# Kernel optimization log

Hardware: AMD Instinct MI355X
Metric: run time of the kernel (lower is better)

## Reference

```python
import jax, jax.numpy as jnp
import numpy as np

B, S, D = 8, 4096, 1024
E = 64            # num_experts
K = 2             # top-k
CAP_F = 1.25      # capacity_factor
TEMP = 0.1        # temperature buffer
Z_COEF = 1e-4
LB_COEF = 1e-4


def setup_inputs() -> dict:
    key = jax.random.key(0)
    kx, k1, k2 = jax.random.split(key, 3)
    x = jax.random.normal(kx, (B, S, D), dtype=jnp.float32)
    W1 = jax.random.normal(k1, (D, D // 2), dtype=jnp.float32) * 0.02
    ln_gamma = jnp.ones((D // 2,), dtype=jnp.float32)
    ln_beta = jnp.zeros((D // 2,), dtype=jnp.float32)
    W2 = jax.random.normal(k2, (D // 2, E), dtype=jnp.float32) * 0.02
    return {"x": x, "W1": W1, "ln_gamma": ln_gamma, "ln_beta": ln_beta, "W2": W2}


def _router_logits(x2, W1, ln_gamma, ln_beta, W2):
    h = x2 @ W1                                   # [T, D//2]
    mu = h.mean(-1, keepdims=True)
    var = h.var(-1, keepdims=True)                # biased var, as torch LayerNorm
    h = (h - mu) / jnp.sqrt(var + 1e-5) * ln_gamma + ln_beta
    h = jax.nn.relu(h)
    logits = h @ W2                               # [T, E]
    logits = jnp.clip(logits, -50.0, 50.0)
    nrm = jnp.linalg.norm(logits, axis=-1, keepdims=True)
    return logits / (jnp.maximum(nrm, 1e-6) + 1e-6)


def reference(x, W1, ln_gamma, ln_beta, W2):
    T = x.shape[0] * x.shape[1]
    x2 = x.reshape(T, -1)
    logits = _router_logits(x2, W1, ln_gamma, ln_beta, W2)   # [T, E]
    routing_weights = jax.nn.softmax(logits / TEMP, axis=-1)

    # top-k + weight renormalization (no_grad in original)
    tw, ti = jax.lax.top_k(routing_weights, K)               # [T, K]
    tw = jnp.clip(tw, 1e-3, 0.8)
    tw = tw / (jnp.maximum(tw.sum(-1, keepdims=True), 1e-6) + 1e-6)
    tw = jax.lax.stop_gradient(tw)
    ti = jax.lax.stop_gradient(ti)

    capacity = CAP_F * T * K / E
    counts = jnp.zeros((E,), dtype=jnp.float32)
    dispatch = jnp.zeros((T, E), dtype=jnp.float32)
    rows = jnp.arange(T)
    for kk in range(K):  # fixed small loop over k, matches sequential scatter semantics
        e = ti[:, kk]                                        # [T] expert ids
        m = counts[e] < capacity                             # capacity check vs pre-step counts
        counts = counts + jax.ops.segment_sum(m.astype(jnp.float32), e, num_segments=E)
        cur = dispatch[rows, e]
        dispatch = dispatch.at[rows, e].set(jnp.where(m, tw[:, kk], cur))

    unrouted = dispatch.sum(-1) == 0                         # [T]
    least_loaded = jnp.argmax(capacity - counts)
    dispatch = jnp.where(unrouted[:, None] & (jnp.arange(E) == least_loaded)[None, :], 1.0, dispatch)
    ndm = dispatch / jnp.maximum(dispatch.sum(-1, keepdims=True), 1e-12)
    ndm = jax.lax.stop_gradient(ndm)

    # training losses
    lp = jnp.clip(jax.nn.log_softmax(logits, axis=-1), -50.0, 50.0)
    z_loss = jnp.minimum(jnp.mean(lp * lp), 100.0)
    usage = ndm.sum(0)
    usage = usage / (jnp.maximum(usage.sum(), 1e-6) + 1e-6)
    usage = jnp.clip(usage, 1e-6, 1.0)
    target = jnp.full((E,), 1.0 / E, dtype=jnp.float32)
    # F.kl_div(log(usage+1e-6), target, reduction='batchmean') on 1-D -> divide by E
    kl = jnp.sum(target * (jnp.log(target) - jnp.log(usage + 1e-6))) / E
    kl = jnp.minimum(kl, 100.0)
    loss = Z_COEF * z_loss + LB_COEF * kl
    loss = jnp.where(jnp.isnan(loss) | jnp.isinf(loss), jnp.float32(0.1), loss)

    return jax.lax.stop_gradient(routing_weights), ndm, loss
```

## Files before the change

### kernel.cpp

```cpp
#include <hip/hip_runtime.h>
#include <hip/hip_bf16.h>
#include <math.h>

#define T_TOK 32768
#define D_IN  1024
#define H_DIM 512
#define N_E   64
#define TM    32
#define BK    16
#define CAPACITY 1280
#define MARGIN   2e-4f
#define MARGIN_F 1e-4f
#define KC1 384

#define WS_H    0ull
#define WS_W1P  67108864ull
#define WS_OFF  69206016ull
#define WS_NEED 69900000ull
#define WS_TI0 0
#define WS_TI1 (4*T_TOK)
#define WS_TW0 (8*T_TOK)
#define WS_TW1 (12*T_TOK)
#define WS_CNT (16*T_TOK)
#define WS_USG (WS_CNT+256)
#define WS_FLAGN (WS_USG+256)
#define WS_ZP  (WS_FLAGN+256)
#define WS_FLAGL (WS_ZP+4096)

typedef __attribute__((ext_vector_type(8))) short short8;
typedef __attribute__((ext_vector_type(4))) float f32x4;

__device__ __forceinline__ float wred64(float v){
#pragma unroll
  for (int m=1;m<64;m<<=1) v += __shfl_xor(v, m, 64);
  return v;
}
__device__ __forceinline__ unsigned short f2bf(float f){
  union { __hip_bfloat16 h; unsigned short u; } cv;
  cv.h = __float2bfloat16(f);
  return cv.u;
}
__device__ __forceinline__ float bf2f(unsigned short u){
  union { __hip_bfloat16 h; unsigned short u; } cv;
  cv.u = u;
  return __bfloat162float(cv.h);
}

__device__ __forceinline__ float np_sum8acc(const float* a, int n){
  float r0=a[0],r1=a[1],r2=a[2],r3=a[3],r4=a[4],r5=a[5],r6=a[6],r7=a[7];
  int lim = n - (n & 7);
  int i = 8;
  for (; i < lim; i += 8){
    r0=__fadd_rn(r0,a[i]);   r1=__fadd_rn(r1,a[i+1]);
    r2=__fadd_rn(r2,a[i+2]); r3=__fadd_rn(r3,a[i+3]);
    r4=__fadd_rn(r4,a[i+4]); r5=__fadd_rn(r5,a[i+5]);
    r6=__fadd_rn(r6,a[i+6]); r7=__fadd_rn(r7,a[i+7]);
  }
  float res=__fadd_rn(__fadd_rn(__fadd_rn(r0,r1),__fadd_rn(r2,r3)),
                      __fadd_rn(__fadd_rn(r4,r5),__fadd_rn(r6,r7)));
  for (; i < n; ++i) res=__fadd_rn(res,a[i]);
  return res;
}
__device__ __forceinline__ float np_sum512(const float* a){
  float s01=__fadd_rn(np_sum8acc(a,128),     np_sum8acc(a+128,128));
  float s23=__fadd_rn(np_sum8acc(a+256,128), np_sum8acc(a+384,128));
  return __fadd_rn(s01,s23);
}

__global__ void k_pack(const float* __restrict__ W1, unsigned short* __restrict__ W1p)
{
  int T = blockIdx.x*256 + threadIdx.x;
  int lane = T & 63;  int rest = T >> 6;
  int nt = rest & 7;  rest >>= 3;
  int s  = rest & 1;  rest >>= 1;
  int ks = rest & 31; int nb = rest >> 5;
  int n  = nb*128 + nt*16 + (lane & 15);
  int kb = ks*32 + (lane >> 4)*8;
  unsigned short o[8];
#pragma unroll
  for (int j=0;j<8;++j){
    float w = W1[(size_t)(kb+j)*H_DIM + n];
    unsigned short hi = f2bf(w);
    o[j] = s ? f2bf(w - bf2f(hi)) : hi;
  }
  size_t base = ((size_t)((((nb*32+ks)*2+s)*8+nt))*512 + (size_t)lane*8);
#pragma unroll
  for (int j=0;j<8;++j) W1p[base+j] = o[j];
}

__launch_bounds__(256)
__global__ void k_g1(const float* __restrict__ x, const unsigned short* __restrict__ W1p,
                     float* __restrict__ h)
{
  __shared__ __align__(16) unsigned short aF[2][8192];
  __shared__ __align__(16) unsigned short bF[2][8192];

  int b = blockIdx.x;
  int logical = (b & 7)*128 + (b >> 3);
  const int nbn = logical >> 8;
  const int bm  = logical & 255;
  const int t0  = bm * 128;

  const int tid  = threadIdx.x;
  const int lane = tid & 63;
  const int wid  = tid >> 6;
  const int wr4  = (wid >> 1) * 4;
  const int wc4  = (wid & 1) * 4;
  const int kq    = tid & 7;
  const int rbase = tid >> 3;
  const int alane = (rbase & 15) + 16*(kq>>1);
  const int j4 = (kq & 1)*4;

  f32x4 acc[4][4];
#pragma unroll
  for (int m=0;m<4;++m)
#pragma unroll
    for (int n=0;n<4;++n) acc[m][n] = (f32x4){0.f,0.f,0.f,0.f};

  {
    float4 xa[4]; uint4 bb[4];
#pragma unroll
    for (int i=0;i<4;++i)
      xa[i] = *(const float4*)&x[(size_t)(t0 + rbase + 32*i)*D_IN + kq*4];
    size_t chunk = (size_t)(nbn*32 + 0) * 8192;
#pragma unroll
    for (int i=0;i<4;++i)
      bb[i] = *(const uint4*)&W1p[chunk + (size_t)(i*256+tid)*8];
#pragma unroll
    for (int i=0;i<4;++i){
      int mt = (rbase + 32*i) >> 4;
      ushort4 uh, ul;
      uh.x=f2bf(xa[i].x); ul.x=f2bf(xa[i].x - bf2f(uh.x));
      uh.y=f2bf(xa[i].y); ul.y=f2bf(xa[i].y - bf2f(uh.y));
      uh.z=f2bf(xa[i].z); ul.z=f2bf(xa[i].z - bf2f(uh.z));
      uh.w=f2bf(xa[i].w); ul.w=f2bf(xa[i].w - bf2f(uh.w));
      *(ushort4*)&aF[0][(mt*64+alane)*8 + j4]        = uh;
      *(ushort4*)&aF[0][4096 + (mt*64+alane)*8 + j4] = ul;
    }
#pragma unroll
    for (int i=0;i<4;++i)
      *(uint4*)&bF[0][(i*256+tid)*8] = bb[i];
  }

  int cur = 0;
  for (int ks=0; ks<32; ++ks){
    __syncthreads();
    float4 xa[4]; uint4 bb[4];
    const bool pre = (ks+1 < 32);
    if (pre){
      int k1 = (ks+1)*32;
#pragma unroll
      for (int i=0;i<4;++i)
        xa[i] = *(const float4*)&x[(size_t)(t0 + rbase + 32*i)*D_IN + k1 + kq*4];
      size_t chunk = (size_t)(nbn*32 + (ks+1)) * 8192;
#pragma unroll
      for (int i=0;i<4;++i)
        bb[i] = *(const uint4*)&W1p[chunk + (size_t)(i*256+tid)*8];
    }
    short8 ah[4], al[4], bh[4], bl[4];
#pragma unroll
    for (int m=0;m<4;++m){
      ah[m] = *(const short8*)&aF[cur][((wr4+m)*64+lane)*8];
      al[m] = *(const short8*)&aF[cur][4096 + ((wr4+m)*64+lane)*8];
    }
#pragma unroll
    for (int n=0;n<4;++n){
      bh[n] = *(const short8*)&bF[cur][((wc4+n)*64+lane)*8];
      bl[n] = *(const short8*)&bF[cur][4096 + ((wc4+n)*64+lane)*8];
    }
#pragma unroll
    for (int m=0;m<4;++m)
#pragma unroll
      for (int n=0;n<4;++n){
        acc[m][n] = __builtin_amdgcn_mfma_f32_16x16x32_bf16(ah[m], bh[n], acc[m][n], 0,0,0);
        acc[m][n] = __builtin_amdgcn_mfma_f32_16x16x32_bf16(al[m], bh[n], acc[m][n], 0,0,0);
        acc[m][n] = __builtin_amdgcn_mfma_f32_16x16x32_bf16(ah[m], bl[n], acc[m][n], 0,0,0);
      }
    if (pre){
      int nb_ = cur ^ 1;
#pragma unroll
      for (int i=0;i<4;++i){
        int mt = (rbase + 32*i) >> 4;
        ushort4 uh, ul;
        uh.x=f2bf(xa[i].x); ul.x=f2bf(xa[i].x - bf2f(uh.x));
        uh.y=f2bf(xa[i].y); ul.y=f2bf(xa[i].y - bf2f(uh.y));
        uh.z=f2bf(xa[i].z); ul.z=f2bf(xa[i].z - bf2f(uh.z));
        uh.w=f2bf(xa[i].w); ul.w=f2bf(xa[i].w - bf2f(uh.w));
        *(ushort4*)&aF[nb_][(mt*64+alane)*8 + j4]        = uh;
        *(ushort4*)&aF[nb_][4096 + (mt*64+alane)*8 + j4] = ul;
      }
#pragma unroll
      for (int i=0;i<4;++i)
        *(uint4*)&bF[nb_][(i*256+tid)*8] = bb[i];
    }
    cur ^= 1;
  }

  const int cr = (lane >> 4) * 4;
  const int cc = lane & 15;
#pragma unroll
  for (int m=0;m<4;++m)
#pragma unroll
    for (int n=0;n<4;++n){
      int row0 = t0 + (wr4+m)*16 + cr;
      int col  = nbn*128 + (wc4+n)*16 + cc;
#pragma unroll
      for (int r=0;r<4;++r)
        h[(size_t)(row0+r)*H_DIM + col] = acc[m][n][r];
    }
}

__launch_bounds__(256, 3)
__global__ void k_ln2(const float* __restrict__ h,
                      const float* __restrict__ gamma,
                      const float* __restrict__ beta,
                      const float* __restrict__ W2,
                      float* __restrict__ out_rw,
                      int*   __restrict__ ti0, int* __restrict__ ti1,
                      float* __restrict__ tw0, float* __restrict__ tw1,
                      float* __restrict__ zpart,
                      int* __restrict__ flagn, int* __restrict__ flagl)
{
  __shared__ __align__(16) char smem[53888];
  __shared__ float zw[4];
  float* hnT  = (float*)smem;
  float* redS = (float*)(smem + 36864);
  float* redQ = (float*)(smem + 36864 + 4224);
  float* sW2  = (float*)(smem + 36864);
  float* logitsL = (float*)(smem + 45312);
  float* muA  = (float*)(smem + 53632);
  float* rsA  = (float*)(smem + 53760);

  const int tid  = threadIdx.x;
  const int wv   = tid >> 6;
  const int lane = tid & 63;
  const int tl   = lane & 7;
  const int cl   = lane >> 3;
  const int cbase = wv*128 + cl*16;
  const int t0 = blockIdx.x * TM;

  float acc[4][16];
#pragma unroll
  for (int j=0;j<4;++j)
#pragma unroll
    for (int q=0;q<4;++q)
      *(float4*)&acc[j][q*4] = *(const float4*)&h[(size_t)(t0+tl*4+j)*H_DIM + cbase + q*4];

  const int g = wv*8 + cl;
#pragma unroll
  for (int j=0;j<4;++j) {
    float s=0.f, qq=0.f;
#pragma unroll
    for (int q=0;q<16;++q){ s += acc[j][q]; qq += acc[j][q]*acc[j][q]; }
    redS[(tl*4+j)*33 + g] = s;
    redQ[(tl*4+j)*33 + g] = qq;
  }
  __syncthreads();
  if (tid < 32) {
    float s=0.f, qq=0.f;
    for (int gg=0; gg<32; ++gg){ s += redS[tid*33+gg]; qq += redQ[tid*33+gg]; }
    float mu = s * (1.f/512.f);
    float var = qq * (1.f/512.f) - mu*mu;
    muA[tid] = mu;
    rsA[tid] = rsqrtf(var + 1e-5f);
  }
  __syncthreads();

  {
    float gmv[16], btv[16];
#pragma unroll
    for (int q=0;q<4;++q){
      *(float4*)&gmv[q*4] = *(const float4*)&gamma[cbase+q*4];
      *(float4*)&btv[q*4] = *(const float4*)&beta[cbase+q*4];
    }
    float mu_[4], rs_[4];
#pragma unroll
    for (int j=0;j<4;++j){ mu_[j]=muA[tl*4+j]; rs_[j]=rsA[tl*4+j]; }
#pragma unroll
    for (int j=0;j<4;++j)
#pragma unroll
      for (int q=0;q<16;++q){
        float hv = (acc[j][q]-mu_[j])*rs_[j]*gmv[q] + btv[q];
        acc[j][q] = fmaxf(hv, 0.f);
      }
  }

  float plog[8];
#pragma unroll
  for (int i=0;i<8;++i) plog[i]=0.f;
  const int t2 = tid & 31, e0 = (tid >> 5) * 8;

  for (int p=0; p<2; ++p) {
    if ((wv>>1) == p) {
      int ccb = (wv&1)*128 + cl*16;
#pragma unroll
      for (int j=0;j<4;++j)
#pragma unroll
        for (int q=0;q<16;++q)
          hnT[(ccb+q)*33 + tl*4 + j] = acc[j][q];
    }
    __syncthreads();
    for (int ch=0; ch<8; ++ch) {
      {
        const float4* src = (const float4*)(W2 + (size_t)(p*256+ch*32)*N_E);
        float4* dst = (float4*)sW2;
        dst[tid]     = src[tid];
        dst[tid+256] = src[tid+256];
      }
      __syncthreads();
#pragma unroll
      for (int kk=0; kk<32; ++kk) {
        float hh = hnT[(ch*32+kk)*33 + t2];
        float4 wa = *(const float4*)&sW2[kk*64 + e0];
        float4 wb = *(const float4*)&sW2[kk*64 + e0 + 4];
        plog[0]=fmaf(hh,wa.x,plog[0]); plog[1]=fmaf(hh,wa.y,plog[1]);
        plog[2]=fmaf(hh,wa.z,plog[2]); plog[3]=fmaf(hh,wa.w,plog[3]);
        plog[4]=fmaf(hh,wb.x,plog[4]); plog[5]=fmaf(hh,wb.y,plog[5]);
        plog[6]=fmaf(hh,wb.z,plog[6]); plog[7]=fmaf(hh,wb.w,plog[7]);
      }
      __syncthreads();
    }
  }
#pragma unroll
  for (int i=0;i<8;++i) logitsL[t2*65 + e0 + i] = plog[i];
  __syncthreads();

  const int tE = tid >> 3, jE = tid & 7;
  float v[8];
#pragma unroll
  for (int i=0;i<8;++i){
    float z = logitsL[tE*65 + jE*8 + i];
    v[i] = fminf(fmaxf(z, -50.f), 50.f);
  }
  float ss = 0.f;
#pragma unroll
  for (int i=0;i<8;++i) ss += v[i]*v[i];
#pragma unroll
  for (int m=1;m<8;m<<=1) ss += __shfl_xor(ss, m, 8);
  float scale = 1.f/(fmaxf(sqrtf(ss), 1e-6f) + 1e-6f);
  float ln[8];
#pragma unroll
  for (int i=0;i<8;++i) ln[i] = v[i]*scale;
  float mx = -1e30f;
#pragma unroll
  for (int i=0;i<8;++i) mx = fmaxf(mx, ln[i]);
#pragma unroll
  for (int m=1;m<8;m<<=1) mx = fmaxf(mx, __shfl_xor(mx, m, 8));

  float ex[8], st=0.f, sn=0.f;
#pragma unroll
  for (int i=0;i<8;++i){
    ex[i] = expf((ln[i]-mx)*10.f);
    st += ex[i];
    sn += expf(ln[i]-mx);
  }
#pragma unroll
  for (int m=1;m<8;m<<=1){ st += __shfl_xor(st, m, 8); sn += __shfl_xor(sn, m, 8); }

  float inv_st = 1.f/st;
  float rw[8];
#pragma unroll
  for (int i=0;i<8;++i) rw[i] = ex[i]*inv_st;

  const size_t tok = (size_t)t0 + tE;
  {
    float4* o = (float4*)(out_rw + tok*N_E + jE*8);
    o[0] = make_float4(rw[0],rw[1],rw[2],rw[3]);
    o[1] = make_float4(rw[4],rw[5],rw[6],rw[7]);
  }

  float g1,g2,g3; int i1,i2;
  {
    float bv=-1e30f; int bi=1<<30;
#pragma unroll
    for (int i=0;i<8;++i){ int idx=jE*8+i;
      if (ln[i]>bv || (ln[i]==bv && idx<bi)){ bv=ln[i]; bi=idx; } }
#pragma unroll
    for (int m=1;m<8;m<<=1){ float ov=__shfl_xor(bv,m,8); int oi=__shfl_xor(bi,m,8);
      if (ov>bv || (ov==bv && oi<bi)){ bv=ov; bi=oi; } }
    g1=bv; i1=bi;
    bv=-1e30f; bi=1<<30;
#pragma unroll
    for (int i=0;i<8;++i){ int idx=jE*8+i; if (idx==i1) continue;
      if (ln[i]>bv || (ln[i]==bv && idx<bi)){ bv=ln[i]; bi=idx; } }
#pragma unroll
    for (int m=1;m<8;m<<=1){ float ov=__shfl_xor(bv,m,8); int oi=__shfl_xor(bi,m,8);
      if (ov>bv || (ov==bv && oi<bi)){ bv=ov; bi=oi; } }
    g2=bv; i2=bi;
    bv=-1e30f;
#pragma unroll
    for (int i=0;i<8;++i){ int idx=jE*8+i; if (idx==i1||idx==i2) continue;
      bv = fmaxf(bv, ln[i]); }
#pragma unroll
    for (int m=1;m<8;m<<=1) bv = fmaxf(bv, __shfl_xor(bv,m,8));
    g3=bv;
  }
  if (jE==0){
    float r1 = expf((g1-mx)*10.f)*inv_st;
    float r2 = expf((g2-mx)*10.f)*inv_st;
    float a1 = fminf(fmaxf(r1, 0.001f), 0.8f);
    float a2 = fminf(fmaxf(r2, 0.001f), 0.8f);
    float d  = fmaxf(a1+a2, 1e-6f) + 1e-6f;
    ti0[tok]=i1; ti1[tok]=i2; tw0[tok]=a1/d; tw1[tok]=a2/d;
    if ((g1-g2) < MARGIN_F || (g2-g3) < MARGIN_F){
      int p = atomicAdd(flagn, 1);
      flagl[p] = (int)tok;
    }
  }

  float lse = mx + logf(sn);
  float zq = 0.f;
#pragma unroll
  for (int i=0;i<8;++i){
    float lp = fminf(fmaxf(ln[i]-lse, -50.f), 50.f);
    zq += lp*lp;
  }
  zq = wred64(zq);
  if (lane==0) zw[wv] = zq;
  __syncthreads();
  if (tid==0) zpart[blockIdx.x] = zw[0]+zw[1]+zw[2]+zw[3];
}

__launch_bounds__(256, 3)
__global__ void k_main(const float* __restrict__ x,
                       const float* __restrict__ W1,
                       const float* __restrict__ gamma,
                       const float* __restrict__ beta,
                       const float* __restrict__ W2,
                       float* __restrict__ out_rw,
                       int*   __restrict__ ti0, int* __restrict__ ti1,
                       float* __restrict__ tw0, float* __restrict__ tw1,
                       float* __restrict__ zpart,
                       int* __restrict__ flagn, int* __restrict__ flagl)
{
  __shared__ __align__(16) char smem[53888];
  __shared__ float zw[4];
  float* sW   = (float*)smem;
  float* sX   = (float*)(smem + 32768);
  float* hnT  = (float*)smem;
  float* redS = (float*)(smem + 36864);
  float* redQ = (float*)(smem + 36864 + 4224);
  float* sW2  = (float*)(smem + 36864);
  float* logitsL = (float*)(smem + 45312);
  float* muA  = (float*)(smem + 53632);
  float* rsA  = (float*)(smem + 53760);

  const int tid  = threadIdx.x;
  const int wv   = tid >> 6;
  const int lane = tid & 63;
  const int tl   = lane & 7;
  const int cl   = lane >> 3;
  const int cbase = wv*128 + cl*16;
  const int t0 = blockIdx.x * TM;

  float acc[4][16];
#pragma unroll
  for (int j=0;j<4;++j)
#pragma unroll
    for (int q=0;q<16;++q) acc[j][q]=0.f;

  for (int k0 = 0; k0 < D_IN; k0 += BK) {
    {
      const float4* srcw = (const float4*)(W1 + (size_t)k0 * H_DIM);
      float4* dstw = (float4*)sW;
#pragma unroll
      for (int i=0;i<8;++i) dstw[tid + 256*i] = srcw[tid + 256*i];
    }
    {
      int e0 = tid*2;
      int tt = e0 >> 4, kk = e0 & 15;
      float2 xv = *(const float2*)&x[(size_t)(t0+tt)*D_IN + k0 + kk];
      sX[kk*36 + tt]     = xv.x;
      sX[(kk+1)*36 + tt] = xv.y;
    }
    __syncthreads();
#pragma unroll
    for (int kk=0; kk<BK; ++kk) {
      float4 a = *(const float4*)&sX[kk*36 + tl*4];
      float b[16];
#pragma unroll
      for (int q=0;q<4;++q) *(float4*)&b[q*4] = *(const float4*)&sW[kk*512 + cbase + q*4];
      float av[4] = {a.x, a.y, a.z, a.w};
#pragma unroll
      for (int j=0;j<4;++j)
#pragma unroll
        for (int q=0;q<16;++q)
          acc[j][q] = fmaf(av[j], b[q], acc[j][q]);
    }
    __syncthreads();
  }

  const int g = wv*8 + cl;
#pragma unroll
  for (int j=0;j<4;++j) {
    float s=0.f, qq=0.f;
#pragma unroll
    for (int q=0;q<16;++q){ s += acc[j][q]; qq += acc[j][q]*acc[j][q]; }
    redS[(tl*4+j)*33 + g] = s;
    redQ[(tl*4+j)*33 + g] = qq;
  }
  __syncthreads();
  if (tid < 32) {
    float s=0.f, qq=0.f;
    for (int gg=0; gg<32; ++gg){ s += redS[tid*33+gg]; qq += redQ[tid*33+gg]; }
    float mu = s * (1.f/512.f);
    float var = qq * (1.f/512.f) - mu*mu;
    muA[tid] = mu;
    rsA[tid] = rsqrtf(var + 1e-5f);
  }
  __syncthreads();

  {
    float gmv[16], btv[16];
#pragma unroll
    for (int q=0;q<4;++q){
      *(float4*)&gmv[q*4] = *(const float4*)&gamma[cbase+q*4];
      *(float4*)&btv[q*4] = *(const float4*)&beta[cbase+q*4];
    }
    float mu_[4], rs_[4];
#pragma unroll
    for (int j=0;j<4;++j){ mu_[j]=muA[tl*4+j]; rs_[j]=rsA[tl*4+j]; }
#pragma unroll
    for (int j=0;j<4;++j)
#pragma unroll
      for (int q=0;q<16;++q){
        float hv = (acc[j][q]-mu_[j])*rs_[j]*gmv[q] + btv[q];
        acc[j][q] = fmaxf(hv, 0.f);
      }
  }

  float plog[8];
#pragma unroll
  for (int i=0;i<8;++i) plog[i]=0.f;
  const int t2 = tid & 31, e0 = (tid >> 5) * 8;

  for (int p=0; p<2; ++p) {
    if ((wv>>1) == p) {
      int ccb = (wv&1)*128 + cl*16;
#pragma unroll
      for (int j=0;j<4;++j)
#pragma unroll
        for (int q=0;q<16;++q)
          hnT[(ccb+q)*33 + tl*4 + j] = acc[j][q];
    }
    __syncthreads();
    for (int ch=0; ch<8; ++ch) {
      {
        const float4* src = (const float4*)(W2 + (size_t)(p*256+ch*32)*N_E);
        float4* dst = (float4*)sW2;
        dst[tid]     = src[tid];
        dst[tid+256] = src[tid+256];
      }
      __syncthreads();
#pragma unroll
      for (int kk=0; kk<32; ++kk) {
        float hh = hnT[(ch*32+kk)*33 + t2];
        float4 wa = *(const float4*)&sW2[kk*64 + e0];
        float4 wb = *(const float4*)&sW2[kk*64 + e0 + 4];
        plog[0]=fmaf(hh,wa.x,plog[0]); plog[1]=fmaf(hh,wa.y,plog[1]);
        plog[2]=fmaf(hh,wa.z,plog[2]); plog[3]=fmaf(hh,wa.w,plog[3]);
        plog[4]=fmaf(hh,wb.x,plog[4]); plog[5]=fmaf(hh,wb.y,plog[5]);
        plog[6]=fmaf(hh,wb.z,plog[6]); plog[7]=fmaf(hh,wb.w,plog[7]);
      }
      __syncthreads();
    }
  }
#pragma unroll
  for (int i=0;i<8;++i) logitsL[t2*65 + e0 + i] = plog[i];
  __syncthreads();

  const int tE = tid >> 3, jE = tid & 7;
  float v[8];
#pragma unroll
  for (int i=0;i<8;++i){
    float z = logitsL[tE*65 + jE*8 + i];
    v[i] = fminf(fmaxf(z, -50.f), 50.f);
  }
  float ss = 0.f;
#pragma unroll
  for (int i=0;i<8;++i) ss += v[i]*v[i];
#pragma unroll
  for (int m=1;m<8;m<<=1) ss += __shfl_xor(ss, m, 8);
  float scale = 1.f/(fmaxf(sqrtf(ss), 1e-6f) + 1e-6f);
  float ln[8];
#pragma unroll
  for (int i=0;i<8;++i) ln[i] = v[i]*scale;
  float mx = -1e30f;
#pragma unroll
  for (int i=0;i<8;++i) mx = fmaxf(mx, ln[i]);
#pragma unroll
  for (int m=1;m<8;m<<=1) mx = fmaxf(mx, __shfl_xor(mx, m, 8));

  float ex[8], st=0.f, sn=0.f;
#pragma unroll
  for (int i=0;i<8;++i){
    ex[i] = expf((ln[i]-mx)*10.f);
    st += ex[i];
    sn += expf(ln[i]-mx);
  }
#pragma unroll
  for (int m=1;m<8;m<<=1){ st += __shfl_xor(st, m, 8); sn += __shfl_xor(sn, m, 8); }

  float inv_st = 1.f/st;
  float rw[8];
#pragma unroll
  for (int i=0;i<8;++i) rw[i] = ex[i]*inv_st;

  const size_t tok = (size_t)t0 + tE;
  {
    float4* o = (float4*)(out_rw + tok*N_E + jE*8);
    o[0] = make_float4(rw[0],rw[1],rw[2],rw[3]);
    o[1] = make_float4(rw[4],rw[5],rw[6],rw[7]);
  }

  float g1,g2,g3; int i1,i2;
  {
    float bv=-1e30f; int bi=1<<30;
#pragma unroll
    for (int i=0;i<8;++i){ int idx=jE*8+i;
      if (ln[i]>bv || (ln[i]==bv && idx<bi)){ bv=ln[i]; bi=idx; } }
#pragma unroll
    for (int m=1;m<8;m<<=1){ float ov=__shfl_xor(bv,m,8); int oi=__shfl_xor(bi,m,8);
      if (ov>bv || (ov==bv && oi<bi)){ bv=ov; bi=oi; } }
    g1=bv; i1=bi;
    bv=-1e30f; bi=1<<30;
#pragma unroll
    for (int i=0;i<8;++i){ int idx=jE*8+i; if (idx==i1) continue;
      if (ln[i]>bv || (ln[i]==bv && idx<bi)){ bv=ln[i]; bi=idx; } }
#pragma unroll
    for (int m=1;m<8;m<<=1){ float ov=__shfl_xor(bv,m,8); int oi=__shfl_xor(bi,m,8);
      if (ov>bv || (ov==bv && oi<bi)){ bv=ov; bi=oi; } }
    g2=bv; i2=bi;
    bv=-1e30f;
#pragma unroll
    for (int i=0;i<8;++i){ int idx=jE*8+i; if (idx==i1||idx==i2) continue;
      bv = fmaxf(bv, ln[i]); }
#pragma unroll
    for (int m=1;m<8;m<<=1) bv = fmaxf(bv, __shfl_xor(bv,m,8));
    g3=bv;
  }
  if (jE==0){
    float r1 = expf((g1-mx)*10.f)*inv_st;
    float r2 = expf((g2-mx)*10.f)*inv_st;
    float a1 = fminf(fmaxf(r1, 0.001f), 0.8f);
    float a2 = fminf(fmaxf(r2, 0.001f), 0.8f);
    float d  = fmaxf(a1+a2, 1e-6f) + 1e-6f;
    ti0[tok]=i1; ti1[tok]=i2; tw0[tok]=a1/d; tw1[tok]=a2/d;
    if ((g1-g2) < MARGIN || (g2-g3) < MARGIN){
      int p = atomicAdd(flagn, 1);
      flagl[p] = (int)tok;
    }
  }

  float lse = mx + logf(sn);
  float zq = 0.f;
#pragma unroll
  for (int i=0;i<8;++i){
    float lp = fminf(fmaxf(ln[i]-lse, -50.f), 50.f);
    zq += lp*lp;
  }
  zq = wred64(zq);
  if (lane==0) zw[wv] = zq;
  __syncthreads();
  if (tid==0) zpart[blockIdx.x] = zw[0]+zw[1]+zw[2]+zw[3];
}

__launch_bounds__(256, 1)
__global__ void k_fix(const float* __restrict__ x, const float* __restrict__ W1,
                      const float* __restrict__ gamma, const float* __restrict__ beta,
                      const float* __restrict__ W2,
                      const int* __restrict__ flagl, const int* __restrict__ flagn,
                      int* __restrict__ ti0, int* __restrict__ ti1,
                      float* __restrict__ tw0, float* __restrict__ tw1)
{
  __shared__ __align__(16) float sx[D_IN];
  __shared__ __align__(16) float sW[32*H_DIM];
  __shared__ float hS[H_DIM], sqS[H_DIM], hnS[H_DIM];
  __shared__ float sq64[N_E], eS[N_E];
  __shared__ float sc[4];
  const int tid = threadIdx.x;
  const int nf = *flagn;
  for (int it = blockIdx.x; it < nf; it += gridDim.x) {
    const int tok = flagl[it];
    ((float4*)sx)[tid] = ((const float4*)(x + (size_t)tok*D_IN))[tid];
    const int c0 = tid*2;
    float h0=0.f, h1=0.f, a0=0.f, a1=0.f;
    for (int kb=0; kb<D_IN; kb+=32){
      __syncthreads();
      const float4* src = (const float4*)(W1 + (size_t)kb*H_DIM);
#pragma unroll
      for (int i=0;i<16;++i) ((float4*)sW)[tid + 256*i] = src[tid + 256*i];
      __syncthreads();
#pragma unroll 8
      for (int k=0;k<32;++k){
        float xk = sx[kb+k];
        float2 w = *(const float2*)&sW[k*H_DIM + c0];
        a0 = fmaf(xk, w.x, a0); a1 = fmaf(xk, w.y, a1);
      }
      int ke = kb + 32;
      if (ke == 384){ h0 = a0; h1 = a1; a0 = 0.f; a1 = 0.f; }
      else if (ke == 768 || ke == 1024){
        h0 = __fadd_rn(h0, a0); h1 = __fadd_rn(h1, a1); a0 = 0.f; a1 = 0.f;
      }
    }
    hS[c0]=h0; hS[c0+1]=h1;
    __syncthreads();
    if (tid==0) sc[0] = __fdiv_rn(np_sum512(hS), 512.0f);
    __syncthreads();
    float mu = sc[0];
    float d0 = __fsub_rn(h0, mu), d1 = __fsub_rn(h1, mu);
    sqS[c0]   = __fmul_rn(d0,d0);
    sqS[c0+1] = __fmul_rn(d1,d1);
    __syncthreads();
    if (tid==0){
      float var = __fdiv_rn(np_sum512(sqS), 512.0f);
      sc[1] = __fsqrt_rn(__fadd_rn(var, 1e-5f));
    }
    __syncthreads();
    float den = sc[1];
    float2 gm = *(const float2*)&gamma[c0];
    float2 bt = *(const float2*)&beta[c0];
    hnS[c0]   = fmaxf(__fadd_rn(__fmul_rn(__fdiv_rn(d0,den), gm.x), bt.x), 0.f);
    hnS[c0+1] = fmaxf(__fadd_rn(__fmul_rn(__fdiv_rn(d1,den), gm.y), bt.y), 0.f);
    float b0=0.f, b1=0.f;
    for (int half=0; half<2; ++half){
      __syncthreads();
      const float4* src = (const float4*)(W2 + (size_t)(half*256)*N_E);
#pragma unroll
      for (int i=0;i<16;++i) ((float4*)sW)[tid + 256*i] = src[tid + 256*i];
      __syncthreads();
      if (tid < N_E){
        if (half==0){
#pragma unroll 8
          for (int c=0;c<256;++c) b0 = fmaf(hnS[c], sW[c*N_E+tid], b0);
        } else {
#pragma unroll 8
          for (int c=256;c<KC1;++c) b0 = fmaf(hnS[c], sW[(c-256)*N_E+tid], b0);
#pragma unroll 8
          for (int c=KC1;c<H_DIM;++c) b1 = fmaf(hnS[c], sW[(c-256)*N_E+tid], b1);
        }
      }
    }
    float lgf = 0.f;
    if (tid < N_E){
      lgf = __fadd_rn(b0, b1);
      lgf = fminf(fmaxf(lgf, -50.f), 50.f);
      sq64[tid] = __fmul_rn(lgf, lgf);
    }
    __syncthreads();
    if (tid==0){
      float nrm = __fsqrt_rn(np_sum8acc(sq64, 64));
      sc[2] = __fadd_rn(fmaxf(nrm, 1e-6f), 1e-6f);
    }
    __syncthreads();
    if (tid < N_E){
      float nl = __fdiv_rn(lgf, sc[2]);
      float z  = __fdiv_rn(nl, 0.1f);
      float mz = z;
#pragma unroll
      for (int m=1;m<64;m<<=1) mz = fmaxf(mz, __shfl_xor(mz,m,64));
      eS[tid] = expf(__fsub_rn(z, mz));
    }
    __syncthreads();
    if (tid==0) sc[3] = np_sum8acc(eS, 64);
    __syncthreads();
    if (tid < N_E){
      float rw = __fdiv_rn(eS[tid], sc[3]);
      float bv = rw; int bi = tid;
#pragma unroll
      for (int m=1;m<64;m<<=1){ float ov=__shfl_xor(bv,m,64); int oi=__shfl_xor(bi,m,64);
        if (ov>bv || (ov==bv && oi<bi)){ bv=ov; bi=oi; } }
      float R1=bv; int I1=bi;
      bv = (tid==I1) ? -1.f : rw; bi = (tid==I1) ? (1<<30) : tid;
#pragma unroll
      for (int m=1;m<64;m<<=1){ float ov=__shfl_xor(bv,m,64); int oi=__shfl_xor(bi,m,64);
        if (ov>bv || (ov==bv && oi<bi)){ bv=ov; bi=oi; } }
      float R2=bv; int I2=bi;
      if (tid==0){
        float A1 = fminf(fmaxf(R1, 0.001f), 0.8f);
        float A2 = fminf(fmaxf(R2, 0.001f), 0.8f);
        float dd = __fadd_rn(fmaxf(__fadd_rn(A1,A2), 1e-6f), 1e-6f);
        ti0[tok]=I1; ti1[tok]=I2;
        tw0[tok]=__fdiv_rn(A1,dd); tw1[tok]=__fdiv_rn(A2,dd);
      }
    }
    __syncthreads();
  }
}

__global__ void k_hist(const int* __restrict__ ti0, int* __restrict__ counts)
{
  __shared__ int lh[N_E];
  int tid = threadIdx.x;
  if (tid < N_E) lh[tid] = 0;
  __syncthreads();
  int i = blockIdx.x*256 + tid;
  atomicAdd(&lh[ti0[i]], 1);
  __syncthreads();
  if (tid < N_E) atomicAdd(&counts[tid], lh[tid]);
}

__global__ void k_dispatch(const int* __restrict__ ti0, const int* __restrict__ ti1,
                           const float* __restrict__ tw0, const float* __restrict__ tw1,
                           const int* __restrict__ counts,
                           float* __restrict__ out_ndm, float* __restrict__ usage)
{
  __shared__ float lus[N_E];
  int tid = threadIdx.x;
  if (tid < N_E) lus[tid] = 0.f;
  __syncthreads();
  int gid = blockIdx.x*256 + tid;
  size_t tok = gid >> 3;
  int jE = gid & 7;
  int i0 = ti0[tok], i1 = ti1[tok];
  float w0 = tw0[tok], w1 = tw1[tok];
  float w1m = (counts[i1] < CAPACITY) ? w1 : 0.f;
  float inv = 1.f / fmaxf(w0 + w1m, 1e-12f);
  float vv[8];
#pragma unroll
  for (int i=0;i<8;++i){
    int e = jE*8+i;
    vv[i] = (e==i0) ? w0*inv : (e==i1) ? w1m*inv : 0.f;
  }
  float4* o = (float4*)(out_ndm + tok*N_E + jE*8);
  o[0] = make_float4(vv[0],vv[1],vv[2],vv[3]);
  o[1] = make_float4(vv[4],vv[5],vv[6],vv[7]);
  if (jE==0){
    atomicAdd(&lus[i0], w0*inv);
    atomicAdd(&lus[i1], w1m*inv);
  }
  __syncthreads();
  if (tid < N_E) atomicAdd(&usage[tid], lus[tid]);
}

__global__ void k_final(const float* __restrict__ usage, const float* __restrict__ zpart,
                        float* __restrict__ out_loss)
{
  int e = threadIdx.x;
  float u = usage[e];
  float usum = wred64(u);
  float un = u / (fmaxf(usum, 1e-6f) + 1e-6f);
  un = fminf(fmaxf(un, 1e-6f), 1.0f);
  const float target = 1.0f/64.0f;
  float term = target * (logf(target) - logf(un + 1e-6f));
  float kl = wred64(term) * (1.0f/64.0f);
  kl = fminf(kl, 100.f);
  float zs = 0.f;
  for (int i=e; i<1024; i+=64) zs += zpart[i];
  zs = wred64(zs);
  float z = fminf(zs / (float)(T_TOK*N_E), 100.f);
  float loss = 1e-4f*z + 1e-4f*kl;
  if (isnan(loss) || isinf(loss)) loss = 0.1f;
  if (e==0) out_loss[0] = loss;
}

extern "C" void kernel_launch(void* const* d_in, const int* in_sizes, int n_in,
                              void* d_out, int out_size, void* d_ws, size_t ws_size,
                              hipStream_t stream) {
  const float* x     = (const float*)d_in[0];
  const float* W1    = (const float*)d_in[1];
  const float* gamma = (const float*)d_in[2];
  const float* beta  = (const float*)d_in[3];
  const float* W2    = (const float*)d_in[4];
  float* out = (float*)d_out;

  const bool fast = (ws_size >= WS_NEED);
  char* ws = (char*)d_ws;
  char* sb = ws + (fast ? WS_OFF : 0ull);
  int*   ti0   = (int*)(sb + WS_TI0);
  int*   ti1   = (int*)(sb + WS_TI1);
  float* tw0   = (float*)(sb + WS_TW0);
  float* tw1   = (float*)(sb + WS_TW1);
  int*   cnts  = (int*)(sb + WS_CNT);
  float* usage = (float*)(sb + WS_USG);
  int*   flagn = (int*)(sb + WS_FLAGN);
  float* zpart = (float*)(sb + WS_ZP);
  int*   flagl = (int*)(sb + WS_FLAGL);

  hipMemsetAsync(sb + WS_CNT, 0, 768, stream);

  float* out_rw   = out;
  float* out_ndm  = out + (size_t)T_TOK*N_E;
  float* out_loss = out + 2ull*T_TOK*N_E;

  if (fast) {
    float* hbuf = (float*)(ws + WS_H);
    unsigned short* W1p = (unsigned short*)(ws + WS_W1P);
    k_pack<<<512, 256, 0, stream>>>(W1, W1p);
    k_g1<<<1024, 256, 0, stream>>>(x, W1p, hbuf);
    k_ln2<<<T_TOK/TM, 256, 0, stream>>>(hbuf, gamma, beta, W2,
                                        out_rw, ti0, ti1, tw0, tw1, zpart,
                                        flagn, flagl);
  } else {
    k_main<<<T_TOK/TM, 256, 0, stream>>>(x, W1, gamma, beta, W2,
                                         out_rw, ti0, ti1, tw0, tw1, zpart,
                                         flagn, flagl);
  }
  k_fix<<<1024, 256, 0, stream>>>(x, W1, gamma, beta, W2, flagl, flagn,
                                  ti0, ti1, tw0, tw1);
  k_hist<<<T_TOK/256, 256, 0, stream>>>(ti0, cnts);
  k_dispatch<<<(T_TOK*8)/256, 256, 0, stream>>>(ti0, ti1, tw0, tw1, cnts,
                                                out_ndm, usage);
  k_final<<<1, 64, 0, stream>>>(usage, zpart, out_loss);
}
```

Measured before the change: 310.4 us.

## Restructure first GEMM to single-buffered LDS with register prefetch and higher occupancy

The first GEMM kernel now keeps a single LDS buffer for A and B and holds the next tile in registers, loading two k-steps ahead. It sets launch bounds to four blocks per SM, remaps block indices so the four column blocks sharing a row tile run close together, and converts x to hi/lo bf16 as 8-element packed uint4 stores. The aim is to halve LDS use to allow more resident blocks, improve L2 reuse of x, and vectorise LDS writes. In exchange it adds a second barrier per k-step and keeps more prefetch registers live under a tighter register budget.

After: 455.6 us. +46.8%, slower.

```diff
diff --git a/kernel.cpp b/kernel.cpp
--- a/kernel.cpp
+++ b/kernel.cpp
@@ -45,6 +45,14 @@
   cv.u = u;
   return __bfloat162float(cv.h);
 }
+__device__ __forceinline__ void cvt8(const float4 A, const float4 B, uint4 &hi, uint4 &lo){
+  unsigned h0=f2bf(A.x),h1=f2bf(A.y),h2=f2bf(A.z),h3=f2bf(A.w);
+  unsigned h4=f2bf(B.x),h5=f2bf(B.y),h6=f2bf(B.z),h7=f2bf(B.w);
+  unsigned l0=f2bf(A.x-bf2f(h0)),l1=f2bf(A.y-bf2f(h1)),l2=f2bf(A.z-bf2f(h2)),l3=f2bf(A.w-bf2f(h3));
+  unsigned l4=f2bf(B.x-bf2f(h4)),l5=f2bf(B.y-bf2f(h5)),l6=f2bf(B.z-bf2f(h6)),l7=f2bf(B.w-bf2f(h7));
+  hi = make_uint4(h0|(h1<<16), h2|(h3<<16), h4|(h5<<16), h6|(h7<<16));
+  lo = make_uint4(l0|(l1<<16), l2|(l3<<16), l4|(l5<<16), l6|(l7<<16));
+}
 
 __device__ __forceinline__ float np_sum8acc(const float* a, int n){
   float r0=a[0],r1=a[1],r2=a[2],r3=a[3],r4=a[4],r5=a[5],r6=a[6],r7=a[7];
@@ -88,17 +96,16 @@
   for (int j=0;j<8;++j) W1p[base+j] = o[j];
 }
 
-__launch_bounds__(256)
+__launch_bounds__(256, 4)
 __global__ void k_g1(const float* __restrict__ x, const unsigned short* __restrict__ W1p,
                      float* __restrict__ h)
 {
-  __shared__ __align__(16) unsigned short aF[2][8192];
-  __shared__ __align__(16) unsigned short bF[2][8192];
-
-  int b = blockIdx.x;
-  int logical = (b & 7)*128 + (b >> 3);
-  const int nbn = logical >> 8;
-  const int bm  = logical & 255;
+  __shared__ __align__(16) unsigned short aF[8192];
+  __shared__ __align__(16) unsigned short bF[8192];
+
+  const int b   = blockIdx.x;
+  const int nbn = (b >> 3) & 3;
+  const int bm  = (b & 7) + (b >> 5) * 8;
   const int t0  = bm * 128;
 
   const int tid  = threadIdx.x;
@@ -106,10 +113,12 @@
   const int wid  = tid >> 6;
   const int wr4  = (wid >> 1) * 4;
   const int wc4  = (wid & 1) * 4;
-  const int kq    = tid & 7;
-  const int rbase = tid >> 3;
-  const int alane = (rbase & 15) + 16*(kq>>1);
-  const int j4 = (kq & 1)*4;
+
+  const int s0 = tid, s1 = tid + 256;
+  const int row0 = ((s0>>6)<<4) + (s0&15);  const int g0 = (s0>>4)&3;
+  const int row1 = ((s1>>6)<<4) + (s1&15);  const int g1 = (s1>>4)&3;
+  const size_t xoff0 = (size_t)(t0+row0)*D_IN + g0*8;
+  const size_t xoff1 = (size_t)(t0+row1)*D_IN + g1*8;
 
   f32x4 acc[4][4];
 #pragma unroll
@@ -117,84 +126,68 @@
 #pragma unroll
     for (int n=0;n<4;++n) acc[m][n] = (f32x4){0.f,0.f,0.f,0.f};
 
-  {
-    float4 xa[4]; uint4 bb[4];
-#pragma unroll
-    for (int i=0;i<4;++i)
-      xa[i] = *(const float4*)&x[(size_t)(t0 + rbase + 32*i)*D_IN + kq*4];
-    size_t chunk = (size_t)(nbn*32 + 0) * 8192;
-#pragma unroll
-    for (int i=0;i<4;++i)
-      bb[i] = *(const uint4*)&W1p[chunk + (size_t)(i*256+tid)*8];
-#pragma unroll
-    for (int i=0;i<4;++i){
-      int mt = (rbase + 32*i) >> 4;
-      ushort4 uh, ul;
-      uh.x=f2bf(xa[i].x); ul.x=f2bf(xa[i].x - bf2f(uh.x));
-      uh.y=f2bf(xa[i].y); ul.y=f2bf(xa[i].y - bf2f(uh.y));
-      uh.z=f2bf(xa[i].z); ul.z=f2bf(xa[i].z - bf2f(uh.z));
-      uh.w=f2bf(xa[i].w); ul.w=f2bf(xa[i].w - bf2f(uh.w));
-      *(ushort4*)&aF[0][(mt*64+alane)*8 + j4]        = uh;
-      *(ushort4*)&aF[0][4096 + (mt*64+alane)*8 + j4] = ul;
-    }
-#pragma unroll
-    for (int i=0;i<4;++i)
-      *(uint4*)&bF[0][(i*256+tid)*8] = bb[i];
-  }
-
-  int cur = 0;
+  float4 x0a, x0b, x1a, x1b;
+  uint4  bb0, bb1, bb2, bb3;
+
+#define LOADG(KS) do {                                                        \
+    int k0_ = (KS)*32;                                                        \
+    x0a = *(const float4*)&x[xoff0 + k0_];                                    \
+    x0b = *(const float4*)&x[xoff0 + k0_ + 4];                                \
+    x1a = *(const float4*)&x[xoff1 + k0_];                                    \
+    x1b = *(const float4*)&x[xoff1 + k0_ + 4];                                \
+    size_t ch_ = (size_t)(nbn*32 + (KS)) * 8192;                              \
+    bb0 = *(const uint4*)&W1p[ch_ + (size_t)(0*256+tid)*8];                   \
+    bb1 = *(const uint4*)&W1p[ch_ + (size_t)(1*256+tid)*8];                   \
+    bb2 = *(const uint4*)&W1p[ch_ + (size_t)(2*256+tid)*8];                   \
+    bb3 = *(const uint4*)&W1p[ch_ + (size_t)(3*256+tid)*8];                   \
+  } while(0)
+
+#define WRITE() do {                                                          \
+    uint4 hi_, lo_;                                                           \
+    cvt8(x0a, x0b, hi_, lo_);                                                 \
+    *(uint4*)&aF[s0*8]        = hi_;                                          \
+    *(uint4*)&aF[4096 + s0*8] = lo_;                                          \
+    cvt8(x1a, x1b, hi_, lo_);                                                 \
+    *(uint4*)&aF[s1*8]        = hi_;                                          \
+    *(uint4*)&aF[4096 + s1*8] = lo_;                                          \
+    *(uint4*)&bF[(0*256+tid)*8] = bb0;                                        \
+    *(uint4*)&bF[(1*256+tid)*8] = bb1;                                        \
+    *(uint4*)&bF[(2*256+tid)*8] = bb2;                                        \
+    *(uint4*)&bF[(3*256+tid)*8] = bb3;                                        \
+  } while(0)
+
+  LOADG(0);
+  WRITE();
+  LOADG(1);
+  __syncthreads();
+
   for (int ks=0; ks<32; ++ks){
-    __syncthreads();
-    float4 xa[4]; uint4 bb[4];
-    const bool pre = (ks+1 < 32);
-    if (pre){
-      int k1 = (ks+1)*32;
-#pragma unroll
-      for (int i=0;i<4;++i)
-        xa[i] = *(const float4*)&x[(size_t)(t0 + rbase + 32*i)*D_IN + k1 + kq*4];
-      size_t chunk = (size_t)(nbn*32 + (ks+1)) * 8192;
-#pragma unroll
-      for (int i=0;i<4;++i)
-        bb[i] = *(const uint4*)&W1p[chunk + (size_t)(i*256+tid)*8];
-    }
-    short8 ah[4], al[4], bh[4], bl[4];
+    short8 ah[4], al[4], bh4[4], bl4[4];
 #pragma unroll
     for (int m=0;m<4;++m){
-      ah[m] = *(const short8*)&aF[cur][((wr4+m)*64+lane)*8];
-      al[m] = *(const short8*)&aF[cur][4096 + ((wr4+m)*64+lane)*8];
+      ah[m] = *(const short8*)&aF[((wr4+m)*64+lane)*8];
+      al[m] = *(const short8*)&aF[4096 + ((wr4+m)*64+lane)*8];
     }
 #pragma unroll
     for (int n=0;n<4;++n){
-      bh[n] = *(const short8*)&bF[cur][((wc4+n)*64+lane)*8];
-      bl[n] = *(const short8*)&bF[cur][4096 + ((wc4+n)*64+lane)*8];
+      bh4[n] = *(const short8*)&bF[((wc4+n)*64+lane)*8];
+      bl4[n] = *(const short8*)&bF[4096 + ((wc4+n)*64+lane)*8];
     }
 #pragma unroll
     for (int m=0;m<4;++m)
 #pragma unroll
       for (int n=0;n<4;++n){
-        acc[m][n] = __builtin_amdgcn_mfma_f32_16x16x32_bf16(ah[m], bh[n], acc[m][n], 0,0,0);
-        acc[m][n] = __builtin_amdgcn_mfma_f32_16x16x32_bf16(al[m], bh[n], acc[m][n], 0,0,0);
-        acc[m][n] = __builtin_amdgcn_mfma_f32_16x16x32_bf16(ah[m], bl[n], acc[m][n], 0,0,0);
-      }
-    if (pre){
-      int nb_ = cur ^ 1;
-#pragma unroll
-      for (int i=0;i<4;++i){
-        int mt = (rbase + 32*i) >> 4;
-        ushort4 uh, ul;
-        uh.x=f2bf(xa[i].x); ul.x=f2bf(xa[i].x - bf2f(uh.x));
-        uh.y=f2bf(xa[i].y); ul.y=f2bf(xa[i].y - bf2f(uh.y));
-        uh.z=f2bf(xa[i].z); ul.z=f2bf(xa[i].z - bf2f(uh.z));
-        uh.w=f2bf(xa[i].w); ul.w=f2bf(xa[i].w - bf2f(uh.w));
-        *(ushort4*)&aF[nb_][(mt*64+alane)*8 + j4]        = uh;
-        *(ushort4*)&aF[nb_][4096 + (mt*64+alane)*8 + j4] = ul;
-      }
-#pragma unroll
-      for (int i=0;i<4;++i)
-        *(uint4*)&bF[nb_][(i*256+tid)*8] = bb[i];
-    }
-    cur ^= 1;
-  }
+        acc[m][n] = __builtin_amdgcn_mfma_f32_16x16x32_bf16(ah[m], bh4[n], acc[m][n], 0,0,0);
+        acc[m][n] = __builtin_amdgcn_mfma_f32_16x16x32_bf16(al[m], bh4[n], acc[m][n], 0,0,0);
+        acc[m][n] = __builtin_amdgcn_mfma_f32_16x16x32_bf16(ah[m], bl4[n], acc[m][n], 0,0,0);
+      }
+    __syncthreads();
+    if (ks < 31) WRITE();
+    if (ks < 30) LOADG(ks+2);
+    __syncthreads();
+  }
+#undef LOADG
+#undef WRITE
 
   const int cr = (lane >> 4) * 4;
   const int cc = lane & 15;
@@ -202,11 +195,11 @@
   for (int m=0;m<4;++m)
 #pragma unroll
     for (int n=0;n<4;++n){
-      int row0 = t0 + (wr4+m)*16 + cr;
-      int col  = nbn*128 + (wc4+n)*16 + cc;
+      int row0_ = t0 + (wr4+m)*16 + cr;
+      int col   = nbn*128 + (wc4+n)*16 + cc;
 #pragma unroll
       for (int r=0;r<4;++r)
-        h[(size_t)(row0+r)*H_DIM + col] = acc[m][n][r];
+        h[(size_t)(row0_+r)*H_DIM + col] = acc[m][n][r];
     }
 }
 
```
